# Kernel tuning notes

Measured on AMD Instinct MI355X. Metric: run time of the kernel, lower is better.

Reference implementation:

```python
import jax, jax.numpy as jnp
import numpy as np

B, H, W, C = 128, 8, 32, 512
RNN = 512; EMB = 512; ATT = 512
VOCAB = 110          # vocab_size -> classes = VOCAB + 1
MAXLEN = 30          # loop runs MAXLEN + 1 steps


def setup_inputs() -> dict:
    key = jax.random.key(0)
    ks = jax.random.split(key, 16)
    w = lambda i, shape: jax.random.normal(ks[i], shape, jnp.float32) * 0.02
    return {
        "features": jax.random.normal(ks[0], (B, H, W, C), jnp.float32),
        "holistic": jax.random.normal(ks[1], (B, RNN), jnp.float32),
        "gt": jax.random.randint(ks[2], (B, MAXLEN + 1), 0, VOCAB + 1),
        "embed_W": w(3, (VOCAB + 1, EMB)),
        "k0": w(4, (EMB, 4 * RNN)), "rk0": w(5, (RNN, 4 * RNN)), "b0": jnp.zeros((4 * RNN,), jnp.float32),
        "k1": w(6, (RNN, 4 * RNN)), "rk1": w(7, (RNN, 4 * RNN)), "b1": jnp.zeros((4 * RNN,), jnp.float32),
        "Wh": w(8, (RNN, ATT)),                       # 1x1 conv on (B,1,1,RNN) == dense
        "Wf": w(9, (3, 3, C, ATT)), "bf": jnp.zeros((ATT,), jnp.float32),
        "wa": w(10, (ATT, 1)),                        # 1x1 conv -> scalar attention logit
        "out_W": w(11, (2 * RNN, VOCAB + 1)), "out_b": jnp.zeros((VOCAB + 1,), jnp.float32),
    }


def _lstm(x, h, c, k, rk, b):
    # Keras LSTMCell: gates order i, f, g(cell), o
    z = x @ k + h @ rk + b
    i, f, g, o = jnp.split(z, 4, axis=-1)
    c2 = jax.nn.sigmoid(f) * c + jax.nn.sigmoid(i) * jnp.tanh(g)
    h2 = jax.nn.sigmoid(o) * jnp.tanh(c2)
    return h2, c2


def reference(features, holistic, gt, embed_W, k0, rk0, b0, k1, rk1, b1,
              Wh, Wf, bf, wa, out_W, out_b):
    Bb, Hh, Ww, Cc = features.shape
    # features_projector (3x3 conv, SAME) is timestep-invariant: precompute once
    fproj = jax.lax.conv_general_dilated(
        features, Wf, (1, 1), "SAME",
        dimension_numbers=("NHWC", "HWIO", "NHWC")) + bf          # (B,H,W,ATT)

    zeros = jnp.zeros((Bb, RNN), features.dtype)
    # prime stacked LSTM with holistic vector (zero initial state)
    h0, c0 = _lstm(holistic, zeros, zeros, k0, rk0, b0)
    h1, c1 = _lstm(h0, zeros, zeros, k1, rk1, b1)

    # teacher forcing: step 0 uses SOS token = vocab_size+1 (out-of-range -> zero one-hot),
    # step t>0 uses gt[:, t-1]
    sos = jnp.full((1, Bb), VOCAB + 1, gt.dtype)
    symbols = jnp.concatenate([sos, gt[:, :MAXLEN].T], axis=0)     # (T, B), T = MAXLEN+1

    def step(carry, sym):
        h0, c0, h1, c1 = carry
        x = jax.nn.one_hot(sym, VOCAB + 1, dtype=features.dtype) @ embed_W   # (B, EMB)
        h0, c0 = _lstm(x, h0, c0, k0, rk0, b0)
        h1, c1 = _lstm(h0, h1, c1, k1, rk1, b1)
        # attention over conv feature map
        hp = h1 @ Wh                                               # (B, ATT)
        proj = jnp.tanh(fproj + hp[:, None, None, :])              # (B,H,W,ATT)
        att = (proj @ wa).reshape(Bb, Hh * Ww)                     # (B, H*W)
        att = jax.nn.softmax(att, axis=-1).reshape(Bb, Hh, Ww, 1)
        glimpse = jnp.sum(features * att, axis=(1, 2))             # (B, C)
        logits = jnp.concatenate([h1, glimpse], axis=-1) @ out_W + out_b
        return (h0, c0, h1, c1), logits

    _, logits = jax.lax.scan(step, (h0, c0, h1, c1), symbols)      # (T, B, VOCAB+1)
    return jnp.transpose(logits, (1, 0, 2))                        # (B, T, VOCAB+1)
```

## Files before the change

### kernel.cpp

```cpp
#include <hip/hip_runtime.h>


typedef __bf16 bf16;
typedef bf16 bf16x8 __attribute__((ext_vector_type(8)));
typedef float f32x4 __attribute__((ext_vector_type(4)));

#define MFMA16(a, b, c) __builtin_amdgcn_mfma_f32_16x16x32_bf16((a), (b), (c), 0, 0, 0)

__device__ __forceinline__ float b2f(unsigned short u) {
    return __uint_as_float(((unsigned int)u) << 16);
}
__device__ __forceinline__ unsigned short f2b(float f) {
    unsigned int x = __float_as_uint(f);
    unsigned int r = (x + 0x7fffu + ((x >> 16) & 1u)) >> 16;
    return (unsigned short)r;
}
__device__ __forceinline__ float exp2_raw(float x) {
    float r;
    asm("v_exp_f32 %0, %1" : "=v"(r) : "v"(x));
    return r;
}
__device__ __forceinline__ float tanh_fast(float x) {
    const float e = exp2_raw(2.885390082f * x);
    return 1.0f - 2.0f * __builtin_amdgcn_rcpf(e + 1.0f);
}
__device__ __forceinline__ float sig_fast(float x) {
    return __builtin_amdgcn_rcpf(1.0f + exp2_raw(-1.44269504f * x));
}
__device__ __forceinline__ void gl16(const ushort* g, ushort* l) {
    __builtin_amdgcn_global_load_lds(
        (const __attribute__((address_space(1))) void*)g,
        (__attribute__((address_space(3))) void*)l, 16, 0, 0);
}
__device__ __forceinline__ float ld_any(const void* p, size_t i, int f32) {
    return f32 ? ((const float*)p)[i] : b2f(((const ushort*)p)[i]);
}

__global__ void detect_dtype(const void* __restrict__ feat, int* __restrict__ flag) {
    if (threadIdx.x == 0 && blockIdx.x == 0) {
        const ushort* u = (const ushort*)feat;
        int cnt = 0;
        for (int i = 0; i < 128; i += 2) {
            const int e = (u[i] >> 7) & 0xFF;
            if (e >= 96 && e <= 150) ++cnt;
        }
        *flag = (cnt >= 40) ? 0 : 1;
    }
}

__global__ __launch_bounds__(256) void setup_misc(
    const void* holistic, const void* embed_W, const void* b0, const void* b1,
    const void* bfv, const void* wa, const void* outB,
    ushort* holB, ushort* embB, float* b0f, float* b1f,
    float* bff, float* waf, float* outBf, const int* __restrict__ flag) {
    const int i = blockIdx.x * 256 + threadIdx.x;
    const int f32 = *flag;
    if (i < 65536) { holB[i] = f2b(ld_any(holistic, i, f32)); return; }
    int j = i - 65536;
    if (j < 56832) { embB[j] = f2b(ld_any(embed_W, j, f32)); return; }
    j -= 56832;
    if (j < 2048) { b0f[j] = ld_any(b0, j, f32); return; }
    j -= 2048;
    if (j < 2048) { b1f[j] = ld_any(b1, j, f32); return; }
    j -= 2048;
    if (j < 512) { bff[j] = ld_any(bfv, j, f32); return; }
    j -= 512;
    if (j < 512) { waf[j] = ld_any(wa, j, f32); return; }
    j -= 512;
    if (j < 111) { outBf[j] = ld_any(outB, j, f32); return; }
}

__global__ __launch_bounds__(256) void build_featpad(
    const void* __restrict__ feat, ushort* __restrict__ featPad,
    const int* __restrict__ flag) {
    const int i = blockIdx.x * 256 + threadIdx.x;
    if (i >= 128 * 10 * 34 * 512) return;
    const int c = i & 511;
    const int xy = i >> 9;
    const int x = xy % 34;
    const int t2 = xy / 34;
    const int y = t2 % 10;
    const int b = t2 / 10;
    ushort v = 0;
    if (y >= 1 && y <= 8 && x >= 1 && x <= 32) {
        const size_t si = ((size_t)((b * 8 + y - 1) * 32 + (x - 1)) << 9) + c;
        v = *flag ? f2b(((const float*)feat)[si]) : ((const ushort*)feat)[si];
    }
    featPad[i] = v;
}

__device__ __forceinline__ void transpose_body(
    const void* in, ushort* out, int R, int C, int bid, int f32) {
    __shared__ float s[32][33];
    const int nbc = C >> 5;
    const int rb = bid / nbc, cb = bid % nbc;
    const int tx = threadIdx.x & 31, ty = threadIdx.x >> 5;
#pragma unroll
    for (int k = 0; k < 4; ++k) {
        const size_t idx = (size_t)(rb * 32 + ty + k * 8) * C + cb * 32 + tx;
        s[ty + k * 8][tx] = f32 ? ((const float*)in)[idx] : b2f(((const ushort*)in)[idx]);
    }
    __syncthreads();
#pragma unroll
    for (int k = 0; k < 4; ++k)
        out[(size_t)(cb * 32 + ty + k * 8) * R + rb * 32 + tx] = f2b(s[tx][ty + k * 8]);
}

__global__ __launch_bounds__(256) void transpose_all(
    const void* k0, const void* rk0, const void* k1, const void* rk1,
    const void* Wh, const void* Wf,
    ushort* k0T, ushort* rk0T, ushort* k1T, ushort* rk1T,
    ushort* WhT, ushort* WfT, const int* __restrict__ flag) {
    const int f32 = *flag;
    const int bid = blockIdx.x;
    if (bid < 1024)      transpose_body(k0, k0T, 512, 2048, bid, f32);
    else if (bid < 2048) transpose_body(rk0, rk0T, 512, 2048, bid - 1024, f32);
    else if (bid < 3072) transpose_body(k1, k1T, 512, 2048, bid - 2048, f32);
    else if (bid < 4096) transpose_body(rk1, rk1T, 512, 2048, bid - 3072, f32);
    else if (bid < 4352) transpose_body(Wh, WhT, 512, 512, bid - 4096, f32);
    else                 transpose_body(Wf, WfT, 4608, 512, bid - 4352, f32);
}

__global__ __launch_bounds__(256) void woT_build_any(
    const void* __restrict__ outW, ushort* __restrict__ WoTpad,
    const int* __restrict__ flag) {
    const int i = blockIdx.x * 256 + threadIdx.x;
    if (i >= 131072) return;
    const int v = i >> 10, k = i & 1023;
    WoTpad[i] = (v < 111) ? f2b(ld_any(outW, (size_t)k * 111 + v, *flag)) : (ushort)0;
}

__global__ __launch_bounds__(256) void conv_fproj(
    const ushort* __restrict__ featPad, const ushort* __restrict__ WfT,
    const float* __restrict__ bff, ushort* __restrict__ fproj) {
    __shared__ __align__(16) ushort As[128 * 64];
    __shared__ __align__(16) ushort Bs[128 * 64];
    const int tid = threadIdx.x;
    const int nb = blockIdx.x >> 8;
    const int rb = blockIdx.x & 255;
    const int b = rb >> 1, p0 = (rb & 1) << 7;
    const int w = tid >> 6, lane = tid & 63, l15 = lane & 15, q = lane >> 4;
    const int wr = (w >> 1) << 6, wc = (w & 1) << 6;
    const int chunkoff = (((lane & 7) ^ (lane >> 3)) << 3);
    int aoff[4], boff[4];
#pragma unroll
    for (int i = 0; i < 4; ++i) {
        const int r = w * 32 + (lane >> 3) + i * 8;
        const int p = p0 + r;
        const int yy = p >> 5, xx = p & 31;
        aoff[i] = (((b * 10 + yy) * 34 + xx) << 9) + chunkoff;
        boff[i] = (nb * 128 + r) * 4608 + chunkoff;
    }
    const int swa = l15 & 7;
    f32x4 acc[4][4] = {};
    for (int kb = 0; kb < 72; ++kb) {
        const int tap = kb >> 3;
        const int dy = tap / 3, dx = tap - dy * 3;
        const int koffA = ((dy * 34 + dx) << 9) + ((kb & 7) << 6);
        const int koffB = kb * 64;
        __syncthreads();
#pragma unroll
        for (int i = 0; i < 4; ++i) {
            gl16(featPad + aoff[i] + koffA, &As[(w * 32 + i * 8) * 64]);
            gl16(WfT + boff[i] + koffB, &Bs[(w * 32 + i * 8) * 64]);
        }
        __syncthreads();
#pragma unroll
        for (int ks = 0; ks < 64; ks += 32) {
            const int cq = (ks >> 3) + q;
            const int col = ((cq ^ swa) << 3);
            bf16x8 af[4], bfr[4];
#pragma unroll
            for (int i = 0; i < 4; ++i) af[i] = *(const bf16x8*)&As[(wr + i * 16 + l15) * 64 + col];
#pragma unroll
            for (int j = 0; j < 4; ++j) bfr[j] = *(const bf16x8*)&Bs[(wc + j * 16 + l15) * 64 + col];
#pragma unroll
            for (int i = 0; i < 4; ++i)
#pragma unroll
                for (int j = 0; j < 4; ++j)
                    acc[i][j] = MFMA16(af[i], bfr[j], acc[i][j]);
        }
    }
    const int rowbase = rb * 128 + wr, colbase = nb * 128 + wc;
#pragma unroll
    for (int i = 0; i < 4; ++i)
#pragma unroll
        for (int j = 0; j < 4; ++j)
#pragma unroll
            for (int rr = 0; rr < 4; ++rr) {
                const int row = rowbase + i * 16 + q * 4 + rr;
                const int col = colbase + j * 16 + l15;
                fproj[(size_t)row * 512 + col] =
                    f2b(2.885390082f * (acc[i][j][rr] + bff[col]));
            }
}

__global__ __launch_bounds__(256) void gemm_bt(
    const ushort* __restrict__ A, const ushort* __restrict__ BT,
    float* __restrict__ C, int M, int N, int K, int lda) {
    __shared__ __align__(16) bf16 As[128][72];
    __shared__ __align__(16) bf16 Bs[128][72];
    const int tid = threadIdx.x;
    const int nnb = N >> 7;
    const int rb = blockIdx.x / nnb, nb = blockIdx.x % nnb;
    const int ar = tid >> 1, ah = (tid & 1) << 5;
    const int w = tid >> 6, lane = tid & 63, l15 = lane & 15, q = lane >> 4;
    const int wr = (w >> 1) << 6, wc = (w & 1) << 6;
    const int r_glob = rb * 128 + ar;
    const bool aval = (r_glob < M);
    const int r_ld = aval ? r_glob : 0;
    f32x4 acc[4][4] = {};
    const int nkb = K >> 6;
    for (int kb = 0; kb < nkb; ++kb) {
        const uint4 z4 = {0u, 0u, 0u, 0u};
        const uint4* asrc = (const uint4*)(A + (size_t)r_ld * lda + kb * 64 + ah);
        uint4 a0 = asrc[0], a1 = asrc[1], a2 = asrc[2], a3 = asrc[3];
        if (!aval) { a0 = z4; a1 = z4; a2 = z4; a3 = z4; }
        const uint4* bsrc = (const uint4*)(BT + (size_t)(nb * 128 + ar) * K + kb * 64 + ah);
        uint4 b0v = bsrc[0], b1v = bsrc[1], b2v = bsrc[2], b3v = bsrc[3];
        __syncthreads();
        *(uint4*)&As[ar][ah] = a0;
        *(uint4*)&As[ar][ah + 8] = a1;
        *(uint4*)&As[ar][ah + 16] = a2;
        *(uint4*)&As[ar][ah + 24] = a3;
        *(uint4*)&Bs[ar][ah] = b0v;
        *(uint4*)&Bs[ar][ah + 8] = b1v;
        *(uint4*)&Bs[ar][ah + 16] = b2v;
        *(uint4*)&Bs[ar][ah + 24] = b3v;
        __syncthreads();
#pragma unroll
        for (int ks = 0; ks < 64; ks += 32) {
            bf16x8 af[4], bfr[4];
#pragma unroll
            for (int i = 0; i < 4; ++i) af[i] = *(const bf16x8*)&As[wr + i * 16 + l15][ks + q * 8];
#pragma unroll
            for (int j = 0; j < 4; ++j) bfr[j] = *(const bf16x8*)&Bs[wc + j * 16 + l15][ks + q * 8];
#pragma unroll
            for (int i = 0; i < 4; ++i)
#pragma unroll
                for (int j = 0; j < 4; ++j)
                    acc[i][j] = MFMA16(af[i], bfr[j], acc[i][j]);
        }
    }
#pragma unroll
    for (int i = 0; i < 4; ++i)
#pragma unroll
        for (int j = 0; j < 4; ++j)
#pragma unroll
            for (int rr = 0; rr < 4; ++rr) {
                const int row = rb * 128 + wr + i * 16 + q * 4 + rr;
                const int col = nb * 128 + wc + j * 16 + l15;
                if (row < M) C[(size_t)row * N + col] = acc[i][j][rr];
            }
}

__global__ __launch_bounds__(256) void lstm_stage(
    int t,
    const ushort* __restrict__ holistic, const int* __restrict__ gt,
    const float* __restrict__ b0f, const float* __restrict__ b1f,
    const ushort* __restrict__ k0T, const ushort* __restrict__ rk0T,
    const ushort* __restrict__ k1T, const ushort* __restrict__ rk1T,
    const float* __restrict__ E0,
    ushort* h0b0, ushort* h0b1, ushort* h1b0, ushort* h1b1,
    float* c0buf, float* c1buf, ushort* HG) {
    const int part = blockIdx.x >> 7;
    const int bi = blockIdx.x & 127;
    const ushort *A1 = nullptr, *A2 = nullptr, *B1 = nullptr, *B2 = nullptr;
    const float* bias = nullptr;
    ushort *hout = nullptr, *hout2 = nullptr;
    float* cbuf = nullptr;
    bool useC = false, useE = false;
    if (part == 0) {
        if (!(t == -2 || (t >= 0 && t <= 30))) return;
        bias = b0f; cbuf = c0buf;
        if (t == -2) { A1 = holistic; B1 = k0T; hout = h0b1; }
        else {
            A1 = ((t + 1) & 1) ? h0b1 : h0b0;
            B1 = rk0T;
            hout = (t & 1) ? h0b1 : h0b0;
            useC = true; useE = true;
        }
    } else {
        if (!(t == -1 || (t >= 1 && t <= 31))) return;
        bias = b1f; cbuf = c1buf;
        if (t == -1) { A1 = h0b1; B1 = k1T; hout = h1b1; }
        else {
            const int s = t - 1;
            A1 = (s & 1) ? h0b1 : h0b0;
            A2 = ((s + 1) & 1) ? h1b1 : h1b0;
            B1 = k1T; B2 = rk1T;
            hout = (s & 1) ? h1b1 : h1b0;
            hout2 = HG + (size_t)s * 131072;
            useC = true;
        }
    }
    const int m0 = (bi >> 5) << 5;
    const int cc0 = (bi & 31) << 4;
    const int tid = threadIdx.x;
    const int w = tid >> 6, lane = tid & 63, l15 = lane & 15, q = lane >> 4;
    __shared__ __align__(16) ushort As1[32 * 520];
    __shared__ __align__(16) ushort As2[32 * 520];
    __shared__ float zs[4][32][17];
#pragma unroll
    for (int it = 0; it < 8; ++it) {
        const int idx = tid + it * 256;
        const int row = idx >> 6, chv = idx & 63;
        *(uint4*)&As1[row * 520 + chv * 8] =
            *(const uint4*)(A1 + (size_t)(m0 + row) * 512 + chv * 8);
    }
    if (A2) {
#pragma unroll
        for (int it = 0; it < 8; ++it) {
            const int idx = tid + it * 256;
            const int row = idx >> 6, chv = idx & 63;
            *(uint4*)&As2[row * 520 + chv * 8] =
                *(const uint4*)(A2 + (size_t)(m0 + row) * 512 + chv * 8);
        }
    }
    __syncthreads();
    const int nkb = A2 ? 16 : 8;
    const size_t brow = (size_t)(w * 512 + cc0 + l15) * 512 + q * 8;
    auto bp = [&](int kb) -> const ushort* {
        const ushort* base = (kb < 8) ? B1 : B2;
        return base + brow + (kb & 7) * 64;
    };
    bf16x8 b0a = *(const bf16x8*)bp(0), b1a = *(const bf16x8*)(bp(0) + 32);
    bf16x8 b0b = *(const bf16x8*)bp(1), b1b = *(const bf16x8*)(bp(1) + 32);
    bf16x8 b0c = *(const bf16x8*)bp(2), b1c = *(const bf16x8*)(bp(2) + 32);
    f32x4 acc0 = {}, acc1 = {};
    for (int kb = 0; kb < nkb; ++kb) {
        const bf16x8 p0 = b0a, p1 = b1a;
        b0a = b0b; b1a = b1b; b0b = b0c; b1b = b1c;
        if (kb + 3 < nkb) {
            b0c = *(const bf16x8*)bp(kb + 3);
            b1c = *(const bf16x8*)(bp(kb + 3) + 32);
        }
        const ushort* asrc = (kb < 8) ? As1 : As2;
        const int kk = (kb & 7) * 64 + q * 8;
        bf16x8 a00 = *(const bf16x8*)&asrc[l15 * 520 + kk];
        bf16x8 a10 = *(const bf16x8*)&asrc[(16 + l15) * 520 + kk];
        bf16x8 a01 = *(const bf16x8*)&asrc[l15 * 520 + kk + 32];
        bf16x8 a11 = *(const bf16x8*)&asrc[(16 + l15) * 520 + kk + 32];
        acc0 = MFMA16(a00, p0, acc0);
        acc1 = MFMA16(a10, p0, acc1);
        acc0 = MFMA16(a01, p1, acc0);
        acc1 = MFMA16(a11, p1, acc1);
    }
#pragma unroll
    for (int rr = 0; rr < 4; ++rr) {
        zs[w][q * 4 + rr][l15] = acc0[rr];
        zs[w][16 + q * 4 + rr][l15] = acc1[rr];
    }
    __syncthreads();
#pragma unroll
    for (int it = 0; it < 2; ++it) {
        const int e = tid + it * 256;
        const int mm = e >> 4, cc = e & 15;
        const int brow2 = m0 + mm, col = cc0 + cc;
        float zi = zs[0][mm][cc] + bias[col];
        float zf = zs[1][mm][cc] + bias[512 + col];
        float zg = zs[2][mm][cc] + bias[1024 + col];
        float zo = zs[3][mm][cc] + bias[1536 + col];
        if (useE) {
            const int s = (t == 0) ? 111 : gt[brow2 * 31 + t - 1];
            if (s >= 0 && s < 111) {
                const float* er = E0 + (size_t)s * 2048;
                zi += er[col]; zf += er[512 + col]; zg += er[1024 + col]; zo += er[1536 + col];
            }
        }
        const float cp = useC ? cbuf[brow2 * 512 + col] : 0.0f;
        const float c2 = sig_fast(zf) * cp + sig_fast(zi) * tanh_fast(zg);
        const float h = sig_fast(zo) * tanh_fast(c2);
        cbuf[brow2 * 512 + col] = c2;
        hout[brow2 * 512 + col] = f2b(h);
        if (hout2) hout2[brow2 * 1024 + col] = f2b(h);
    }
}

__global__ __launch_bounds__(256) void att_logits(
    const ushort* __restrict__ fproj, const float* __restrict__ HP,
    const float* __restrict__ waf, float* __restrict__ attL) {
    __shared__ float hpS[8][512];
    __shared__ float waS[512];
    __shared__ float accS[128][9];
    const int tid = threadIdx.x;
    const int b = blockIdx.x >> 3, ph = (blockIdx.x >> 2) & 1, th = blockIdx.x & 3;
    const int t0 = th << 3, tc = (th == 3) ? 7 : 8;
    const int pl = tid & 127, ch = tid >> 7;
    const int p = ph * 128 + pl;
    for (int i = tid; i < 8 * 512; i += 256) {
        const int tt = i >> 9, c = i & 511;
        hpS[tt][c] = (tt < tc) ? 2.885390082f * HP[((size_t)(t0 + tt) * 128 + b) * 512 + c] : 0.0f;
    }
    waS[tid] = -2.0f * waf[tid];
    if (tid < 256) waS[256 + tid] = -2.0f * waf[256 + tid];
    __syncthreads();
    float sumW = 0.f;
    {
        const float* wh = &waS[ch * 256];
        for (int c4 = 0; c4 < 64; ++c4) {
            const float4 wv = *(const float4*)&wh[c4 * 4];
            sumW += wv.x + wv.y + wv.z + wv.w;
        }
        sumW *= -0.5f;
    }
    float acc[8];
#pragma unroll
    for (int tt = 0; tt < 8; ++tt) acc[tt] = 0.f;
    const ushort* frow = fproj + (size_t)(b * 256 + p) * 512 + ch * 256;
    for (int c8 = 0; c8 < 32; ++c8) {
        const int cc = ch * 256 + c8 * 8;
        const uint4 fv = *(const uint4*)(frow + c8 * 8);
        float f[8];
        f[0] = b2f((unsigned short)(fv.x & 0xffff)); f[1] = b2f((unsigned short)(fv.x >> 16));
        f[2] = b2f((unsigned short)(fv.y & 0xffff)); f[3] = b2f((unsigned short)(fv.y >> 16));
        f[4] = b2f((unsigned short)(fv.z & 0xffff)); f[5] = b2f((unsigned short)(fv.z >> 16));
        f[6] = b2f((unsigned short)(fv.w & 0xffff)); f[7] = b2f((unsigned short)(fv.w >> 16));
        const float4 w0 = *(const float4*)&waS[cc];
        const float4 w1 = *(const float4*)&waS[cc + 4];
#pragma unroll
        for (int tt = 0; tt < 8; ++tt) {
            const float4 h0 = *(const float4*)&hpS[tt][cc];
            const float4 h1 = *(const float4*)&hpS[tt][cc + 4];
            float s = acc[tt];
            s = fmaf(__builtin_amdgcn_rcpf(exp2_raw(f[0] + h0.x) + 1.0f), w0.x, s);
            s = fmaf(__builtin_amdgcn_rcpf(exp2_raw(f[1] + h0.y) + 1.0f), w0.y, s);
            s = fmaf(__builtin_amdgcn_rcpf(exp2_raw(f[2] + h0.z) + 1.0f), w0.z, s);
            s = fmaf(__builtin_amdgcn_rcpf(exp2_raw(f[3] + h0.w) + 1.0f), w0.w, s);
            s = fmaf(__builtin_amdgcn_rcpf(exp2_raw(f[4] + h1.x) + 1.0f), w1.x, s);
            s = fmaf(__builtin_amdgcn_rcpf(exp2_raw(f[5] + h1.y) + 1.0f), w1.y, s);
            s = fmaf(__builtin_amdgcn_rcpf(exp2_raw(f[6] + h1.z) + 1.0f), w1.z, s);
            s = fmaf(__builtin_amdgcn_rcpf(exp2_raw(f[7] + h1.w) + 1.0f), w1.w, s);
            acc[tt] = s;
        }
    }
    if (ch == 1) {
#pragma unroll
        for (int tt = 0; tt < 8; ++tt) accS[pl][tt] = acc[tt] + sumW;
    }
    __syncthreads();
    if (ch == 0) {
        for (int tt = 0; tt < tc; ++tt)
            attL[((size_t)(t0 + tt) * 128 + b) * 256 + p] = acc[tt] + sumW + accS[pl][tt];
    }
}

__global__ __launch_bounds__(256) void glimpse_kernel(
    const ushort* __restrict__ featPad, const float* __restrict__ attL,
    ushort* __restrict__ HG) {
    __shared__ __align__(16) float attT[256 * 36];
    const int tid = threadIdx.x;
    const int b = blockIdx.x >> 1, chh = blockIdx.x & 1;
    const int c0 = chh << 8;
    const int w = tid >> 6, lane = tid & 63;
    for (int i = tid; i < 31 * 256; i += 256) {
        const int tt = i >> 8, p = i & 255;
        attT[p * 36 + tt] = attL[((size_t)tt * 128 + b) * 256 + p];
    }
    __syncthreads();
    for (int tt = w; tt < 31; tt += 4) {
        float v0 = attT[lane * 36 + tt], v1 = attT[(lane + 64) * 36 + tt];
        float v2 = attT[(lane + 128) * 36 + tt], v3 = attT[(lane + 192) * 36 + tt];
        float mx = fmaxf(fmaxf(v0, v1), fmaxf(v2, v3));
#pragma unroll
        for (int m = 1; m < 64; m <<= 1) mx = fmaxf(mx, __shfl_xor(mx, m));
        const float e0 = exp2_raw((v0 - mx) * 1.44269504f);
        const float e1 = exp2_raw((v1 - mx) * 1.44269504f);
        const float e2 = exp2_raw((v2 - mx) * 1.44269504f);
        const float e3 = exp2_raw((v3 - mx) * 1.44269504f);
        float s = e0 + e1 + e2 + e3;
#pragma unroll
        for (int m = 1; m < 64; m <<= 1) s += __shfl_xor(s, m);
        const float r = 1.0f / s;
        attT[lane * 36 + tt] = e0 * r;  attT[(lane + 64) * 36 + tt] = e1 * r;
        attT[(lane + 128) * 36 + tt] = e2 * r;  attT[(lane + 192) * 36 + tt] = e3 * r;
    }
    __syncthreads();
    float acc[31];
#pragma unroll
    for (int tt = 0; tt < 31; ++tt) acc[tt] = 0.f;
    for (int p = 0; p < 256; ++p) {
        const size_t fi = (((size_t)(b * 10 + (p >> 5) + 1) * 34 + (p & 31) + 1) << 9) + c0 + tid;
        const float fv = b2f(featPad[fi]);
        const float4 a0 = *(const float4*)&attT[p * 36];
        const float4 a1 = *(const float4*)&attT[p * 36 + 4];
        const float4 a2 = *(const float4*)&attT[p * 36 + 8];
        const float4 a3 = *(const float4*)&attT[p * 36 + 12];
        const float4 a4 = *(const float4*)&attT[p * 36 + 16];
        const float4 a5 = *(const float4*)&attT[p * 36 + 20];
        const float4 a6 = *(const float4*)&attT[p * 36 + 24];
        const float4 a7 = *(const float4*)&attT[p * 36 + 28];
        acc[0] = fmaf(fv, a0.x, acc[0]);   acc[1] = fmaf(fv, a0.y, acc[1]);
        acc[2] = fmaf(fv, a0.z, acc[2]);   acc[3] = fmaf(fv, a0.w, acc[3]);
        acc[4] = fmaf(fv, a1.x, acc[4]);   acc[5] = fmaf(fv, a1.y, acc[5]);
        acc[6] = fmaf(fv, a1.z, acc[6]);   acc[7] = fmaf(fv, a1.w, acc[7]);
        acc[8] = fmaf(fv, a2.x, acc[8]);   acc[9] = fmaf(fv, a2.y, acc[9]);
        acc[10] = fmaf(fv, a2.z, acc[10]); acc[11] = fmaf(fv, a2.w, acc[11]);
        acc[12] = fmaf(fv, a3.x, acc[12]); acc[13] = fmaf(fv, a3.y, acc[13]);
        acc[14] = fmaf(fv, a3.z, acc[14]); acc[15] = fmaf(fv, a3.w, acc[15]);
        acc[16] = fmaf(fv, a4.x, acc[16]); acc[17] = fmaf(fv, a4.y, acc[17]);
        acc[18] = fmaf(fv, a4.z, acc[18]); acc[19] = fmaf(fv, a4.w, acc[19]);
        acc[20] = fmaf(fv, a5.x, acc[20]); acc[21] = fmaf(fv, a5.y, acc[21]);
        acc[22] = fmaf(fv, a5.z, acc[22]); acc[23] = fmaf(fv, a5.w, acc[23]);
        acc[24] = fmaf(fv, a6.x, acc[24]); acc[25] = fmaf(fv, a6.y, acc[25]);
        acc[26] = fmaf(fv, a6.z, acc[26]); acc[27] = fmaf(fv, a6.w, acc[27]);
        acc[28] = fmaf(fv, a7.x, acc[28]); acc[29] = fmaf(fv, a7.y, acc[29]);
        acc[30] = fmaf(fv, a7.z, acc[30]);
    }
#pragma unroll
    for (int tt = 0; tt < 31; ++tt)
        HG[((size_t)tt * 128 + b) * 1024 + 512 + c0 + tid] = f2b(acc[tt]);
}

__global__ __launch_bounds__(256) void logits_store(
    const float* __restrict__ C, const float* __restrict__ outBf,
    void* __restrict__ out, const int* __restrict__ flag) {
    const int i = blockIdx.x * 256 + threadIdx.x;
    if (i >= 3968 * 111) return;
    const int r = i / 111, v = i - r * 111;
    const int tt = r >> 7, b = r & 127;
    const float a = C[(size_t)r * 128 + v] + outBf[v];
    const size_t oi = ((size_t)b * 31 + tt) * 111 + v;
    if (*flag) ((float*)out)[oi] = a;
    else       ((ushort*)out)[oi] = f2b(a);
}

extern "C" void kernel_launch(void* const* d_in, const int* in_sizes, int n_in,
                              void* d_out, int out_size, void* d_ws, size_t ws_size,
                              hipStream_t stream) {
    (void)in_sizes; (void)n_in; (void)out_size;
    const void* features = d_in[0];
    const void* holistic = d_in[1];
    const int*  gt       = (const int*)d_in[2];
    const void* embed_W  = d_in[3];
    const void* k0 = d_in[4];
    const void* rk0 = d_in[5];
    const void* b0 = d_in[6];
    const void* k1 = d_in[7];
    const void* rk1 = d_in[8];
    const void* b1 = d_in[9];
    const void* Wh = d_in[10];
    const void* Wf = d_in[11];
    const void* bfv = d_in[12];
    const void* wa = d_in[13];
    const void* outW = d_in[14];
    const void* outB = d_in[15];

    char* ws = (char*)d_ws;
    size_t off = 0;
    auto take = [&](size_t bytes) -> char* {
        char* p = ws + off;
        off += (bytes + 255) & ~(size_t)255;
        return p;
    };
    int*    flag    = (int*)take(256);
    ushort* featPad = (ushort*)take(128ull * 10 * 34 * 512 * 2);
    ushort* holB  = (ushort*)take(65536ull * 2);
    ushort* embB  = (ushort*)take(56832ull * 2);
    float*  b0f   = (float*)take(2048ull * 4);
    float*  b1f   = (float*)take(2048ull * 4);
    float*  bff   = (float*)take(512ull * 4);
    float*  waf   = (float*)take(512ull * 4);
    float*  outBf = (float*)take(111ull * 4);
    ushort* WoTpad = (ushort*)take(131072ull * 2);
    ushort* fproj = (ushort*)take(32768ull * 512 * 2);
    ushort* WfT   = (ushort*)take(4608ull * 512 * 2);
    ushort* k0T   = (ushort*)take(2048ull * 512 * 2);
    ushort* rk0T  = (ushort*)take(2048ull * 512 * 2);
    ushort* k1T   = (ushort*)take(2048ull * 512 * 2);
    ushort* rk1T  = (ushort*)take(2048ull * 512 * 2);
    ushort* WhT   = (ushort*)take(512ull * 512 * 2);
    float*  E0    = (float*)take(111ull * 2048 * 4);
    ushort* h0b0  = (ushort*)take(128ull * 512 * 2);
    ushort* h0b1  = (ushort*)take(128ull * 512 * 2);
    ushort* h1b0  = (ushort*)take(128ull * 512 * 2);
    ushort* h1b1  = (ushort*)take(128ull * 512 * 2);
    float*  c0buf = (float*)take(128ull * 512 * 4);
    float*  c1buf = (float*)take(128ull * 512 * 4);
    ushort* HG    = (ushort*)take(3968ull * 1024 * 2);
    float*  HP    = (float*)take(3968ull * 512 * 4);
    float*  attL  = (float*)take(31ull * 128 * 256 * 4);
    float*  Cout  = (float*)attL;
    if (off > ws_size) return;

    detect_dtype<<<dim3(1), dim3(64), 0, stream>>>(features, flag);
    build_featpad<<<dim3(87040), dim3(256), 0, stream>>>(features, featPad, flag);
    setup_misc<<<dim3(499), dim3(256), 0, stream>>>(
        holistic, embed_W, b0, b1, bfv, wa, outB,
        holB, embB, b0f, b1f, bff, waf, outBf, flag);
    transpose_all<<<dim3(6656), dim3(256), 0, stream>>>(
        k0, rk0, k1, rk1, Wh, Wf, k0T, rk0T, k1T, rk1T, WhT, WfT, flag);
    woT_build_any<<<dim3(512), dim3(256), 0, stream>>>(outW, WoTpad, flag);
    conv_fproj<<<dim3(1024), dim3(256), 0, stream>>>(featPad, WfT, bff, fproj);
    gemm_bt<<<dim3(16), dim3(256), 0, stream>>>(embB, k0T, E0, 111, 2048, 512, 512);
    for (int t = -2; t <= 31; ++t)
        lstm_stage<<<dim3(256), dim3(256), 0, stream>>>(t, holB, gt, b0f, b1f,
            k0T, rk0T, k1T, rk1T, E0, h0b0, h0b1, h1b0, h1b1, c0buf, c1buf, HG);
    gemm_bt<<<dim3(31 * 4), dim3(256), 0, stream>>>(HG, WhT, HP, 3968, 512, 512, 1024);
    att_logits<<<dim3(1024), dim3(256), 0, stream>>>(fproj, HP, waf, attL);
    glimpse_kernel<<<dim3(256), dim3(256), 0, stream>>>(featPad, attL, HG);
    gemm_bt<<<dim3(31), dim3(256), 0, stream>>>(HG, WoTpad, Cout, 3968, 128, 1024, 1024);
    logits_store<<<dim3(1721), dim3(256), 0, stream>>>(Cout, outBf, d_out, flag);
}
```

Before: 915.2 us.

## Overlap 3x3 conv projection with serial LSTM steps via extra blocks

The standalone conv_fproj kernel is split into K-slices that run as 181 extra blocks in each of the 34 serial LSTM step launches. This lets the compute-heavy conv fill CUs the latency-bound LSTM steps leave idle. Partial sums accumulate into an fp32 fproj buffer across launches, and the bias is applied later in att_logits. This costs more workspace and twice the fproj read bandwidth, and needs a fallback path when the workspace is too small.

```diff
diff --git a/kernel.cpp b/kernel.cpp
--- a/kernel.cpp
+++ b/kernel.cpp
@@ -254,7 +254,7 @@
             }
 }
 
-__global__ __launch_bounds__(256) void lstm_stage(
+__global__ __launch_bounds__(256) void lstm_conv_step(
     int t,
     const ushort* __restrict__ holistic, const int* __restrict__ gt,
     const float* __restrict__ b0f, const float* __restrict__ b1f,
@@ -262,7 +262,79 @@
     const ushort* __restrict__ k1T, const ushort* __restrict__ rk1T,
     const float* __restrict__ E0,
     ushort* h0b0, ushort* h0b1, ushort* h1b0, ushort* h1b1,
-    float* c0buf, float* c1buf, ushort* HG) {
+    float* c0buf, float* c1buf, ushort* HG,
+    const ushort* __restrict__ featPad, const ushort* __restrict__ WfT,
+    float* __restrict__ fprojF, int nslice) {
+    __shared__ __align__(16) ushort smem[37632];
+    const int tid = threadIdx.x;
+    const int w = tid >> 6, lane = tid & 63, l15 = lane & 15, q = lane >> 4;
+
+    if (blockIdx.x >= 256) {
+        const int sid = (t + 2) * nslice + ((int)blockIdx.x - 256);
+        if (sid >= 6144) return;
+        const int tile = sid & 1023, s = sid >> 10;
+        const int nb = tile >> 8, rb = tile & 255;
+        const int b = rb >> 1, p0 = (rb & 1) << 7;
+        ushort* As = smem;
+        ushort* Bs = smem + 8192;
+        const int wr = (w >> 1) << 6, wc = (w & 1) << 6;
+        const int chunkoff = (((lane & 7) ^ (lane >> 3)) << 3);
+        int aoff[4], boff[4];
+#pragma unroll
+        for (int i = 0; i < 4; ++i) {
+            const int r = w * 32 + (lane >> 3) + i * 8;
+            const int p = p0 + r;
+            const int yy = p >> 5, xx = p & 31;
+            aoff[i] = (((b * 10 + yy) * 34 + xx) << 9) + chunkoff;
+            boff[i] = (nb * 128 + r) * 4608 + chunkoff;
+        }
+        const int swa = l15 & 7;
+        f32x4 acc[4][4] = {};
+        const int kb0 = s * 12, kb1 = kb0 + 12;
+        for (int kb = kb0; kb < kb1; ++kb) {
+            const int tap = kb >> 3;
+            const int dy = tap / 3, dx = tap - dy * 3;
+            const int koffA = ((dy * 34 + dx) << 9) + ((kb & 7) << 6);
+            const int koffB = kb * 64;
+            __syncthreads();
+#pragma unroll
+            for (int i = 0; i < 4; ++i) {
+                gl16(featPad + aoff[i] + koffA, &As[(w * 32 + i * 8) * 64]);
+                gl16(WfT + boff[i] + koffB, &Bs[(w * 32 + i * 8) * 64]);
+            }
+            __syncthreads();
+#pragma unroll
+            for (int ks = 0; ks < 64; ks += 32) {
+                const int cq = (ks >> 3) + q;
+                const int col = ((cq ^ swa) << 3);
+                bf16x8 af[4], bfr[4];
+#pragma unroll
+                for (int i = 0; i < 4; ++i) af[i] = *(const bf16x8*)&As[(wr + i * 16 + l15) * 64 + col];
+#pragma unroll
+                for (int j = 0; j < 4; ++j) bfr[j] = *(const bf16x8*)&Bs[(wc + j * 16 + l15) * 64 + col];
+#pragma unroll
+                for (int i = 0; i < 4; ++i)
+#pragma unroll
+                    for (int j = 0; j < 4; ++j)
+                        acc[i][j] = MFMA16(af[i], bfr[j], acc[i][j]);
+            }
+        }
+        const int rowbase = rb * 128 + wr, colbase = nb * 128 + wc;
+#pragma unroll
+        for (int i = 0; i < 4; ++i)
+#pragma unroll
+            for (int j = 0; j < 4; ++j)
+#pragma unroll
+                for (int rr = 0; rr < 4; ++rr) {
+                    const int row = rowbase + i * 16 + q * 4 + rr;
+                    const int col = colbase + j * 16 + l15;
+                    float* d = fprojF + (size_t)row * 512 + col;
+                    if (s == 0) *d = acc[i][j][rr];
+                    else        *d += acc[i][j][rr];
+                }
+        return;
+    }
+
     const int part = blockIdx.x >> 7;
     const int bi = blockIdx.x & 127;
     const ushort *A1 = nullptr, *A2 = nullptr, *B1 = nullptr, *B2 = nullptr;
@@ -296,11 +368,9 @@
     }
     const int m0 = (bi >> 5) << 5;
     const int cc0 = (bi & 31) << 4;
-    const int tid = threadIdx.x;
-    const int w = tid >> 6, lane = tid & 63, l15 = lane & 15, q = lane >> 4;
-    __shared__ __align__(16) ushort As1[32 * 520];
-    __shared__ __align__(16) ushort As2[32 * 520];
-    __shared__ float zs[4][32][17];
+    ushort* As1 = smem;
+    ushort* As2 = smem + 16640;
+    float*  zsf = (float*)(smem + 33280);
 #pragma unroll
     for (int it = 0; it < 8; ++it) {
         const int idx = tid + it * 256;
@@ -348,8 +418,8 @@
     }
 #pragma unroll
     for (int rr = 0; rr < 4; ++rr) {
-        zs[w][q * 4 + rr][l15] = acc0[rr];
-        zs[w][16 + q * 4 + rr][l15] = acc1[rr];
+        zsf[w * 544 + (q * 4 + rr) * 17 + l15] = acc0[rr];
+        zsf[w * 544 + (16 + q * 4 + rr) * 17 + l15] = acc1[rr];
     }
     __syncthreads();
 #pragma unroll
@@ -357,10 +427,10 @@
         const int e = tid + it * 256;
         const int mm = e >> 4, cc = e & 15;
         const int brow2 = m0 + mm, col = cc0 + cc;
-        float zi = zs[0][mm][cc] + bias[col];
-        float zf = zs[1][mm][cc] + bias[512 + col];
-        float zg = zs[2][mm][cc] + bias[1024 + col];
-        float zo = zs[3][mm][cc] + bias[1536 + col];
+        float zi = zsf[0 * 544 + mm * 17 + cc] + bias[col];
+        float zf = zsf[1 * 544 + mm * 17 + cc] + bias[512 + col];
+        float zg = zsf[2 * 544 + mm * 17 + cc] + bias[1024 + col];
+        float zo = zsf[3 * 544 + mm * 17 + cc] + bias[1536 + col];
         if (useE) {
             const int s = (t == 0) ? 111 : gt[brow2 * 31 + t - 1];
             if (s >= 0 && s < 111) {
@@ -378,10 +448,12 @@
 }
 
 __global__ __launch_bounds__(256) void att_logits(
-    const ushort* __restrict__ fproj, const float* __restrict__ HP,
-    const float* __restrict__ waf, float* __restrict__ attL) {
+    const void* __restrict__ fprojP, const float* __restrict__ HP,
+    const float* __restrict__ waf, const float* __restrict__ bff,
+    float* __restrict__ attL, int fpMode) {
     __shared__ float hpS[8][512];
     __shared__ float waS[512];
+    __shared__ float bffS[512];
     __shared__ float accS[128][9];
     const int tid = threadIdx.x;
     const int b = blockIdx.x >> 3, ph = (blockIdx.x >> 2) & 1, th = blockIdx.x & 3;
@@ -393,7 +465,11 @@
         hpS[tt][c] = (tt < tc) ? 2.885390082f * HP[((size_t)(t0 + tt) * 128 + b) * 512 + c] : 0.0f;
     }
     waS[tid] = -2.0f * waf[tid];
-    if (tid < 256) waS[256 + tid] = -2.0f * waf[256 + tid];
+    bffS[tid] = 2.885390082f * bff[tid];
+    if (tid < 256) {
+        waS[256 + tid] = -2.0f * waf[256 + tid];
+        bffS[256 + tid] = 2.885390082f * bff[256 + tid];
+    }
     __syncthreads();
     float sumW = 0.f;
     {
@@ -407,15 +483,29 @@
     float acc[8];
 #pragma unroll
     for (int tt = 0; tt < 8; ++tt) acc[tt] = 0.f;
-    const ushort* frow = fproj + (size_t)(b * 256 + p) * 512 + ch * 256;
+    const ushort* frowB = (const ushort*)fprojP + (size_t)(b * 256 + p) * 512 + ch * 256;
+    const float*  frowF = (const float*)fprojP + (size_t)(b * 256 + p) * 512 + ch * 256;
     for (int c8 = 0; c8 < 32; ++c8) {
         const int cc = ch * 256 + c8 * 8;
-        const uint4 fv = *(const uint4*)(frow + c8 * 8);
         float f[8];
-        f[0] = b2f((unsigned short)(fv.x & 0xffff)); f[1] = b2f((unsigned short)(fv.x >> 16));
-        f[2] = b2f((unsigned short)(fv.y & 0xffff)); f[3] = b2f((unsigned short)(fv.y >> 16));
-        f[4] = b2f((unsigned short)(fv.z & 0xffff)); f[5] = b2f((unsigned short)(fv.z >> 16));
-        f[6] = b2f((unsigned short)(fv.w & 0xffff)); f[7] = b2f((unsigned short)(fv.w >> 16));
+        if (fpMode) {
+            const float4 v0 = *(const float4*)(frowF + c8 * 8);
+            const float4 v1 = *(const float4*)(frowF + c8 * 8 + 4);
+            f[0] = fmaf(2.885390082f, v0.x, bffS[cc + 0]);
+            f[1] = fmaf(2.885390082f, v0.y, bffS[cc + 1]);
+            f[2] = fmaf(2.885390082f, v0.z, bffS[cc + 2]);
+            f[3] = fmaf(2.885390082f, v0.w, bffS[cc + 3]);
+            f[4] = fmaf(2.885390082f, v1.x, bffS[cc + 4]);
+            f[5] = fmaf(2.885390082f, v1.y, bffS[cc + 5]);
+            f[6] = fmaf(2.885390082f, v1.z, bffS[cc + 6]);
+            f[7] = fmaf(2.885390082f, v1.w, bffS[cc + 7]);
+        } else {
+            const uint4 fv = *(const uint4*)(frowB + c8 * 8);
+            f[0] = b2f((unsigned short)(fv.x & 0xffff)); f[1] = b2f((unsigned short)(fv.x >> 16));
+            f[2] = b2f((unsigned short)(fv.y & 0xffff)); f[3] = b2f((unsigned short)(fv.y >> 16));
+            f[4] = b2f((unsigned short)(fv.z & 0xffff)); f[5] = b2f((unsigned short)(fv.z >> 16));
+            f[6] = b2f((unsigned short)(fv.w & 0xffff)); f[7] = b2f((unsigned short)(fv.w >> 16));
+        }
         const float4 w0 = *(const float4*)&waS[cc];
         const float4 w1 = *(const float4*)&waS[cc + 4];
 #pragma unroll
@@ -563,7 +653,6 @@
     float*  waf   = (float*)take(512ull * 4);
     float*  outBf = (float*)take(111ull * 4);
     ushort* WoTpad = (ushort*)take(131072ull * 2);
-    ushort* fproj = (ushort*)take(32768ull * 512 * 2);
     ushort* WfT   = (ushort*)take(4608ull * 512 * 2);
     ushort* k0T   = (ushort*)take(2048ull * 512 * 2);
     ushort* rk0T  = (ushort*)take(2048ull * 512 * 2);
@@ -581,7 +670,12 @@
     float*  HP    = (float*)take(3968ull * 512 * 4);
     float*  attL  = (float*)take(31ull * 128 * 256 * 4);
     float*  Cout  = (float*)attL;
-    if (off > ws_size) return;
+    const size_t fp32Need = 32768ull * 512 * 4;
+    const size_t bf16Need = 32768ull * 512 * 2;
+    const int mainMode = (off + fp32Need <= ws_size) ? 1 : 0;
+    float*  fprojF = (float*)(ws + off);
+    ushort* fprojB = (ushort*)(ws + off);
+    if (!mainMode && off + bf16Need > ws_size) return;
 
     detect_dtype<<<dim3(1), dim3(64), 0, stream>>>(features, flag);
     build_featpad<<<dim3(87040), dim3(256), 0, stream>>>(features, featPad, flag);
@@ -591,13 +685,22 @@
     transpose_all<<<dim3(6656), dim3(256), 0, stream>>>(
         k0, rk0, k1, rk1, Wh, Wf, k0T, rk0T, k1T, rk1T, WhT, WfT, flag);
     woT_build_any<<<dim3(512), dim3(256), 0, stream>>>(outW, WoTpad, flag);
-    conv_fproj<<<dim3(1024), dim3(256), 0, stream>>>(featPad, WfT, bff, fproj);
     gemm_bt<<<dim3(16), dim3(256), 0, stream>>>(embB, k0T, E0, 111, 2048, 512, 512);
-    for (int t = -2; t <= 31; ++t)
-        lstm_stage<<<dim3(256), dim3(256), 0, stream>>>(t, holB, gt, b0f, b1f,
-            k0T, rk0T, k1T, rk1T, E0, h0b0, h0b1, h1b0, h1b1, c0buf, c1buf, HG);
+    if (mainMode) {
+        for (int t = -2; t <= 31; ++t)
+            lstm_conv_step<<<dim3(437), dim3(256), 0, stream>>>(t, holB, gt, b0f, b1f,
+                k0T, rk0T, k1T, rk1T, E0, h0b0, h0b1, h1b0, h1b1, c0buf, c1buf, HG,
+                featPad, WfT, fprojF, 181);
+    } else {
+        conv_fproj<<<dim3(1024), dim3(256), 0, stream>>>(featPad, WfT, bff, fprojB);
+        for (int t = -2; t <= 31; ++t)
+            lstm_conv_step<<<dim3(256), dim3(256), 0, stream>>>(t, holB, gt, b0f, b1f,
+                k0T, rk0T, k1T, rk1T, E0, h0b0, h0b1, h1b0, h1b1, c0buf, c1buf, HG,
+                featPad, WfT, nullptr, 0);
+    }
     gemm_bt<<<dim3(31 * 4), dim3(256), 0, stream>>>(HG, WhT, HP, 3968, 512, 512, 1024);
-    att_logits<<<dim3(1024), dim3(256), 0, stream>>>(fproj, HP, waf, attL);
+    att_logits<<<dim3(1024), dim3(256), 0, stream>>>(
+        mainMode ? (const void*)fprojF : (const void*)fprojB, HP, waf, bff, attL, mainMode);
     glimpse_kernel<<<dim3(256), dim3(256), 0, stream>>>(featPad, attL, HG);
     gemm_bt<<<dim3(31), dim3(256), 0, stream>>>(HG, WoTpad, Cout, 3968, 128, 1024, 1024);
     logits_store<<<dim3(1721), dim3(256), 0, stream>>>(Cout, outBf, d_out, flag);
```

Result: slower. 1.523 ms (+66.4%).
